# Kernel optimization log

Measured on AMD Instinct MI355X. Metric: run time of the kernel, lower is better.

The kernel has to match this reference:

```python
import jax, jax.numpy as jnp
import numpy as np

MUL = 50        # e3nn mul=50 channel multiplicity
LAYERS = 6      # layers=6
NBASIS = 10     # radial basis size
MAXR = 0.06     # max_radius
HIDDEN = 64     # radial MLP hidden
NPATHS = 5      # TP paths: s*Y0->s, s*Y1->v, v.Y1->s, vxY1->v, Y2@v->v
HALF_BAR = 0.05 # half bar length (bar lengths [0.1,0.1,0.1])


def setup_inputs() -> dict:
    key = jax.random.key(0)
    ks = jax.random.split(key, 9)
    B, L = 64, 514
    C = MUL
    y = jax.random.normal(ks[0], (B, L, 6), dtype=jnp.float32) * 0.03
    W_embed = jax.random.normal(ks[1], (3, C), dtype=jnp.float32) / np.sqrt(3.0)
    Wr1 = jax.random.normal(ks[2], (LAYERS, NBASIS + 2, HIDDEN), dtype=jnp.float32) / np.sqrt(NBASIS + 2.0)
    br1 = jnp.zeros((LAYERS, HIDDEN), dtype=jnp.float32)
    Wr2 = jax.random.normal(ks[3], (LAYERS, HIDDEN, NPATHS * C), dtype=jnp.float32) / np.sqrt(float(HIDDEN))
    Ws = jax.random.normal(ks[4], (LAYERS, C, C), dtype=jnp.float32) / np.sqrt(float(C))
    Wv = jax.random.normal(ks[5], (LAYERS, C, C), dtype=jnp.float32) / np.sqrt(float(C))
    Wg = jax.random.normal(ks[6], (LAYERS, C, C), dtype=jnp.float32) / np.sqrt(float(C))
    W_out = jax.random.normal(ks[7], (C,), dtype=jnp.float32) / np.sqrt(float(C))
    return {"y": y, "W_embed": W_embed, "Wr1": Wr1, "br1": br1, "Wr2": Wr2,
            "Ws": Ws, "Wv": Wv, "Wg": Wg, "W_out": W_out}


def _cross2d(a, b):
    return a[..., 0] * b[..., 1] - a[..., 1] * b[..., 0]


def _forward(y, W_embed, Wr1, br1, Wr2, Ws, Wv, Wg, W_out):
    B, L, _ = y.shape
    T = L - 2
    C = MUL
    # --- slinky coord transform: (x, z, alpha) dof -> 9 cartesian points/triplet ---
    ctr = jnp.stack([y[..., 0], y[..., 1]], axis=-1)                 # (B,L,2) bar centers
    a = y[..., 2]
    off = HALF_BAR * jnp.stack([-jnp.sin(a), jnp.cos(a)], axis=-1)   # (B,L,2)
    pts = jnp.stack([ctr + off, ctr, ctr - off], axis=-2)            # (B,L,3,2) top/center/bottom
    trip = jnp.stack([pts[:, :-2], pts[:, 1:-1], pts[:, 2:]], axis=2)  # (B,T,3bars,3pts,2)
    cart = trip.reshape(B * T, 9, 2)
    nt = B * T
    N = nt * 9
    pos = jnp.concatenate([cart.reshape(-1, 2), jnp.zeros((N, 1), cart.dtype)], axis=-1)  # (N,3)
    # --- fixed intra-triplet edge pattern ---
    base = jnp.array([[1, 0], [1, 2], [4, 3], [4, 5], [7, 6], [7, 8], [1, 4], [4, 7]], dtype=jnp.int32)
    eidx = (base[None] + 9 * jnp.arange(nt, dtype=jnp.int32)[:, None, None]).reshape(-1, 2)
    src, dst = eidx[:, 0], eidx[:, 1]
    edge_attr = jnp.tile(jax.nn.one_hot(jnp.array([1, 1, 1, 1, 1, 1, 0, 0]), 2, dtype=pos.dtype), (nt, 1))  # (E,2)
    node_attr = jnp.tile(jax.nn.one_hot(jnp.array([1, 0, 1]), 2, dtype=pos.dtype), (3 * nt, 1))             # (N,2)
    node_input = jnp.ones((N, 1), pos.dtype)
    # --- edge geometry: radial embedding + spherical harmonics l<=2 ---
    edge_vec = pos[src] - pos[dst]
    r = jnp.linalg.norm(edge_vec, axis=-1)
    u = edge_vec / (r[:, None] + 1e-12)                              # Y1 (l=1)
    centers = jnp.linspace(0.0, MAXR, NBASIS)
    width = MAXR / (NBASIS - 1)
    rb = jnp.exp(-jnp.square((r[:, None] - centers) / width))        # (E,NBASIS)
    t = jnp.clip(r / MAXR, 0.0, 1.0)
    fcut = 0.5 * (jnp.cos(jnp.float32(np.pi) * t) + 1.0)             # smooth cutoff at max_radius
    emb = jnp.concatenate([rb * fcut[:, None], edge_attr], axis=-1)  # (E,NBASIS+2)
    Y2 = u[:, :, None] * u[:, None, :] - jnp.eye(3, dtype=u.dtype) / 3.0  # traceless l=2 (E,3,3)
    # --- node feature init: scalars (0e) + zero vectors (1o) ---
    s = jnp.concatenate([node_input, node_attr], axis=-1) @ W_embed  # (N,C)
    v = jnp.zeros((N, C, 3), pos.dtype)
    for l in range(LAYERS):
        w = jax.nn.silu(emb @ Wr1[l] + br1[l]) @ Wr2[l]              # radial MLP -> TP weights
        w = w.reshape(-1, NPATHS, C) * fcut[:, None, None]           # (E,5,C)
        ss, vs = s[src], v[src]
        m_s = w[:, 0] * ss + w[:, 2] * jnp.einsum('ecd,ed->ec', vs, u)
        m_v = (w[:, 1, :, None] * ss[:, :, None] * u[:, None, :]
               + w[:, 3, :, None] * jnp.cross(vs, u[:, None, :])
               + w[:, 4, :, None] * jnp.einsum('ecd,edk->eck', vs, Y2))
        s_agg = jax.ops.segment_sum(m_s, dst, num_segments=N)        # scatter-add (num_neighbors=1)
        v_agg = jax.ops.segment_sum(m_v, dst, num_segments=N)
        h = s + s_agg
        s = jax.nn.silu(h @ Ws[l])                                   # scalar nonlinearity
        gate = jax.nn.sigmoid(h @ Wg[l])                             # equivariant gate for vectors
        v = jnp.einsum('ncd,ck->nkd', v + v_agg, Wv[l]) * gate[:, :, None]
    out = jnp.einsum('ncd,c->nd', v, W_out)                          # 1x1o readout, (N,3)
    output = out.reshape(B, T, 3, 3, 3)                              # (B,T,bar,point,xyz)
    cart_b = cart.reshape(B, T, 3, 3, 2)
    result = jnp.zeros((B, L, 3), y.dtype)
    result = result.at[:, 1:-1, 0:2].set(output.sum(axis=-2)[..., 1, 0:2])
    tmp = (_cross2d(cart_b[..., 0, :] - cart_b[..., 1, :], output[..., 0, 0:2])
           + _cross2d(cart_b[..., 2, :] - cart_b[..., 1, :], output[..., 2, 0:2]))
    result = result.at[:, 1:-1, 2].set(tmp[..., 1])
    return result


def reference(y, W_embed, Wr1, br1, Wr2, Ws, Wv, Wg, W_out):
    return _forward(y, W_embed, Wr1, br1, Wr2, Ws, Wv, Wg, W_out)
```

## Files before the change

### kernel.cpp

```cpp
#include <hip/hip_runtime.h>
#include <math.h>

#define PI_F 3.14159265358979323846f

typedef _Float16 h8 __attribute__((ext_vector_type(8)));
typedef float f4 __attribute__((ext_vector_type(4)));

__device__ __forceinline__ float sigm_(float x){ return 1.0f/(1.0f+__expf(-x)); }
__device__ __forceinline__ float silu_(float x){ return x*sigm_(x); }
__device__ __forceinline__ h8 ldh8(const _Float16* p){
    return __builtin_bit_cast(h8, *(const float4*)(p));
}

#define B1_PER_L 21504
#define B2_PER_L 12288
#define B1_TOT   129024
#define B_TOT    202752

__global__ void precompute_all(const float* __restrict__ W_embed,
                               const float* __restrict__ Wr1,
                               const float* __restrict__ br1,
                               const float* __restrict__ Wr2,
                               const float* __restrict__ Ws,
                               const float* __restrict__ Wg,
                               const float* __restrict__ Wv,
                               float* __restrict__ pre,
                               float* __restrict__ T,
                               int tabN,
                               _Float16* __restrict__ B,
                               float* __restrict__ out,
                               int nTb)
{
    const int bid = blockIdx.x;
    const int tid = threadIdx.x;
    const float wdt = 0.06f / 9.0f;

    if (bid == 0) {
        for (int i = tid; i < 384; i += 256) {
            int b = i / 6, r = i - b * 6;
            int t = (r < 3) ? 0 : 513;
            out[((size_t)(b * 514 + t)) * 3 + (r % 3)] = 0.0f;
        }
        __shared__ float s1[50];
        __shared__ float hid[64];
        if (tid < 50) s1[tid] = W_embed[tid] + W_embed[50 + tid];
        __syncthreads();

        const float rbar = 0.05f;
        const float fcb = 0.5f * (__cosf(PI_F * (rbar / 0.06f)) + 1.0f);
        float emb[12];
#pragma unroll
        for (int i = 0; i < 10; ++i) {
            float d = (rbar - (float)i * wdt) / wdt;
            emb[i] = __expf(-d * d) * fcb;
        }
        emb[10] = 0.0f; emb[11] = 1.0f;

        for (int l = 0; l < 6; ++l) {
            if (tid < 50) pre[l * 50 + tid] = s1[tid];
            if (tid < 64) {
                float a = br1[l * 64 + tid];
#pragma unroll
                for (int i = 0; i < 12; ++i) a += emb[i] * Wr1[l * 768 + i * 64 + tid];
                hid[tid] = silu_(a);
            }
            __syncthreads();
            for (int m = tid; m < 250; m += 256) {
                float acc = 0.0f;
                for (int j = 0; j < 64; ++j) acc += hid[j] * Wr2[l * 16000 + j * 250 + m];
                pre[300 + l * 250 + m] = acc * fcb;
            }
            float sacc = 0.0f;
            if (tid < 50) {
                for (int c = 0; c < 50; ++c) sacc += s1[c] * Ws[l * 2500 + c * 50 + tid];
            }
            __syncthreads();
            if (tid < 50) s1[tid] = silu_(sacc);
            __syncthreads();
        }
    } else if (bid <= nTb) {
        const int e = (bid - 1) * 4 + (tid >> 6);
        const int lane = tid & 63;
        const int total = 6 * (tabN + 1);
        if (e >= total) return;
        const int l = e / (tabN + 1);
        const int i = e - l * (tabN + 1);

        float r = (float)i * (0.06f / (float)tabN);
        float t = fminf(r * (1.0f / 0.06f), 1.0f);
        float fc = 0.5f * (__cosf(PI_F * t) + 1.0f);
        float emb[10];
#pragma unroll
        for (int k = 0; k < 10; ++k) {
            float d = (r - (float)k * wdt) / wdt;
            emb[k] = __expf(-d * d) * fc;
        }
        float a = br1[l * 64 + lane] + Wr1[l * 768 + 640 + lane];
#pragma unroll
        for (int k = 0; k < 10; ++k) a += emb[k] * Wr1[l * 768 + k * 64 + lane];
        float hv = silu_(a);

        float acc0 = 0.0f, acc1 = 0.0f;
        const float* wr2 = Wr2 + l * 16000;
        for (int j = 0; j < 64; ++j) {
            float hj = __shfl(hv, j);
            acc0 += hj * wr2[j * 250 + lane];
            acc1 += hj * wr2[j * 250 + 64 + lane];
        }
        float* tp = T + (size_t)e * 100;
        tp[lane] = acc0 * fc;
        if (lane < 36) tp[64 + lane] = acc1 * fc;
    } else {
        int idx = (bid - 1 - nTb) * 256 + tid;
        if (idx >= B_TOT) return;
        int l, n, k, which;
        size_t off;
        if (idx < B1_TOT) {
            l = idx / B1_PER_L; int r = idx - l * B1_PER_L;
            n = r / 192; k = r - n * 192; which = 0;
            off = (size_t)l * B1_PER_L + n * 192 + k;
        } else {
            int j = idx - B1_TOT;
            l = j / B2_PER_L; int r = j - l * B2_PER_L;
            n = r / 192; k = r - n * 192; which = 1;
            off = B1_TOT + (size_t)l * B2_PER_L + n * 192 + k;
        }
        int seg = -1, c = 0;
        if (k < 50)                  { seg = 0; c = k; }
        else if (k >= 64 && k < 114) { seg = 1; c = k - 64; }
        else if (k >= 128 && k < 178){ seg = 2; c = k - 128; }
        _Float16 val = (_Float16)0.0f;
        if (seg >= 0) {
            float w = 0.0f;
            if (which == 0) {
                if (n < 50)       w = Ws[l * 2500 + c * 50 + n];
                else if (n < 100) w = Wg[l * 2500 + c * 50 + (n - 50)];
            } else {
                if (n < 50)       w = Wv[l * 2500 + c * 50 + n];
            }
            _Float16 hi = (_Float16)w;
            val = (seg < 2) ? hi : (_Float16)(w - (float)hi);
        }
        B[off] = val;
    }
}

__global__ __launch_bounds__(256, 4)
void fused_main(const float* __restrict__ y,
                const float* __restrict__ W_embed,
                const float* __restrict__ W_out,
                const float* __restrict__ pre,
                const float* __restrict__ T,
                int tabN,
                const _Float16* __restrict__ Bws,
                float* __restrict__ out)
{
    __shared__ __align__(16) char LB[112 * 152 * 2];
    _Float16* A   = (_Float16*)LB;
    float* outHT  = (float*)LB;
    float* outQT  = (float*)LB + 3200;

    const int tid  = threadIdx.x;
    const int wave = tid >> 6;
    const int lane = tid & 63;
    const int kl   = (lane < 50) ? lane : 49;
    const int fm   = lane & 15;
    const int fq   = lane >> 4;

    const _Float16* B1 = Bws;
    const _Float16* B2 = Bws + B1_TOT;

    float offx[2], offy[2], u3x_[2], u3y_[2], uspx_[2], uspy_[2], fr_[2];
    int   ti_[2], inr_[2];
#pragma unroll
    for (int w = 0; w < 2; ++w) {
        int wid = blockIdx.x * 8 + wave * 2 + w;
        int b = wid >> 9, tw = wid & 511;
        const float* yb = y + ((size_t)(b * 514 + tw)) * 6;
        float c0x = yb[0], c0y = yb[1];
        float c1x = yb[6], c1y = yb[7], a1 = yb[8];
        float sn, cs; __sincosf(a1, &sn, &cs);
        offx[w] = -0.05f * sn; offy[w] = 0.05f * cs;
        float svx = c0x - c1x, svy = c0y - c1y;
        float r_sp = sqrtf(svx * svx + svy * svy);
        float inv_sp = 1.0f / (r_sp + 1e-12f);
        uspx_[w] = svx * inv_sp; uspy_[w] = svy * inv_sp;
        float rb2 = sqrtf(offx[w] * offx[w] + offy[w] * offy[w]);
        float invb = 1.0f / (rb2 + 1e-12f);
        u3x_[w] = -offx[w] * invb; u3y_[w] = -offy[w] * invb;
        float tp = r_sp * ((float)tabN / 0.06f);
        inr_[w] = tp < (float)tabN;
        int ti = (int)tp;
        if (ti > tabN - 1) ti = tabN - 1;
        if (ti < 0) ti = 0;
        ti_[w] = ti; fr_[w] = tp - (float)ti;
    }

    float s3[2], s4[2], s5[2];
    float v3x[2], v3y[2], v3z[2], v4x[2], v4y[2], v4z[2], v5x[2], v5y[2], v5z[2];
    {
        float i35 = W_embed[kl] + W_embed[100 + kl];
        float i4  = W_embed[kl] + W_embed[50 + kl];
#pragma unroll
        for (int w = 0; w < 2; ++w) {
            s3[w] = i35; s5[w] = i35; s4[w] = i4;
            v3x[w] = v3y[w] = v3z[w] = 0.0f;
            v4x[w] = v4y[w] = v4z[w] = 0.0f;
            v5x[w] = v5y[w] = v5z[w] = 0.0f;
        }
    }

    for (int l = 0; l < 6; ++l) {
        __syncthreads();

        float s1l = pre[l * 50 + kl];
        const float* wbp = pre + 300 + l * 250;
        float wb0 = wbp[kl], wb1 = wbp[50 + kl], wb2 = wbp[100 + kl],
              wb3 = wbp[150 + kl], wb4 = wbp[200 + kl];

        const float THIRD = 1.0f / 3.0f;
#pragma unroll
        for (int w = 0; w < 2; ++w) {
            const float* tb = T + ((size_t)(l * (tabN + 1) + ti_[w])) * 100;
            float t00 = tb[kl], t01 = tb[50 + kl], t10 = tb[100 + kl], t11 = tb[150 + kl];
            float wsp0 = inr_[w] ? (t00 + fr_[w] * (t10 - t00)) : 0.0f;
            float wsp1 = inr_[w] ? (t01 + fr_[w] * (t11 - t01)) : 0.0f;

            float u3x = u3x_[w], u3y = u3y_[w];
            float dot3 = v4x[w] * u3x + v4y[w] * u3y;
            float ms3 = wb0 * s4[w] + wb2 * dot3;
            float ms5 = wb0 * s4[w] - wb2 * dot3;
            float ms4 = wsp0 * s1l;
            float bAx = wb1 * s4[w] * u3x - wb3 * v4z[w] * u3y;
            float bAy = wb1 * s4[w] * u3y + wb3 * v4z[w] * u3x;
            float bBx = wb4 * (dot3 * u3x - v4x[w] * THIRD);
            float bBy = wb4 * (dot3 * u3y - v4y[w] * THIRD);
            float crz = wb3 * (v4x[w] * u3y - v4y[w] * u3x);
            float mzc = -wb4 * v4z[w] * THIRD;

            float vals[12];
            vals[0] = s3[w] + ms3;
            vals[1] = s4[w] + ms4;
            vals[2] = s5[w] + ms5;
            vals[3] = v3x[w] + bAx + bBx;
            vals[4] = v3y[w] + bAy + bBy;
            vals[5] = v3z[w] + crz + mzc;
            vals[6] = v4x[w] + wsp1 * s1l * uspx_[w];
            vals[7] = v4y[w] + wsp1 * s1l * uspy_[w];
            vals[8] = v4z[w];
            vals[9]  = v5x[w] - bAx + bBx;
            vals[10] = v5y[w] - bAy + bBy;
            vals[11] = v5z[w] - crz + mzc;

            int wv = wave * 2 + w;
#pragma unroll
            for (int q = 0; q < 12; ++q) {
                int row = (q < 3) ? (wv * 3 + q) : (32 + wv * 9 + (q - 3));
                float x = (lane < 50) ? vals[q] : 0.0f;
                _Float16 hi = (_Float16)x;
                _Float16 lo = (_Float16)(x - (float)hi);
                A[row * 152 + lane]      = hi;
                A[row * 152 + 64 + lane] = lo;
            }
        }
        {
            int pr  = tid >> 4;
            int row = (pr < 8) ? (24 + pr) : (96 + pr);
            f4 z = {0.0f, 0.0f, 0.0f, 0.0f};
            *(f4*)(A + row * 152 + (tid & 15) * 8) = z;
        }
        __syncthreads();

        f4 cst[9];
        const _Float16* B1l = B1 + (size_t)l * B1_PER_L;
        const _Float16* B2l = B2 + (size_t)l * B2_PER_L;

        {
            const _Float16* bp = B1l + (wave * 16 + fm) * 192 + fq * 8;
            h8 b0 = ldh8(bp), b1 = ldh8(bp + 32), b2 = ldh8(bp + 64),
               b3 = ldh8(bp + 96), b4 = ldh8(bp + 128), b5 = ldh8(bp + 160);
#pragma unroll
            for (int mt = 0; mt < 2; ++mt) {
                const _Float16* ap = A + (mt * 16 + fm) * 152 + fq * 8;
                h8 a0 = ldh8(ap), a1 = ldh8(ap + 32), a2 = ldh8(ap + 64), a3 = ldh8(ap + 96);
                f4 acc = {0.0f, 0.0f, 0.0f, 0.0f};
                acc = __builtin_amdgcn_mfma_f32_16x16x32_f16(a0, b0, acc, 0, 0, 0);
                acc = __builtin_amdgcn_mfma_f32_16x16x32_f16(a1, b1, acc, 0, 0, 0);
                acc = __builtin_amdgcn_mfma_f32_16x16x32_f16(a2, b2, acc, 0, 0, 0);
                acc = __builtin_amdgcn_mfma_f32_16x16x32_f16(a3, b3, acc, 0, 0, 0);
                acc = __builtin_amdgcn_mfma_f32_16x16x32_f16(a0, b4, acc, 0, 0, 0);
                acc = __builtin_amdgcn_mfma_f32_16x16x32_f16(a1, b5, acc, 0, 0, 0);
                cst[mt] = acc;
            }
        }
        if (wave < 3) {
            const _Float16* bp = B1l + ((4 + wave) * 16 + fm) * 192 + fq * 8;
            h8 b0 = ldh8(bp), b1 = ldh8(bp + 32), b2 = ldh8(bp + 64),
               b3 = ldh8(bp + 96), b4 = ldh8(bp + 128), b5 = ldh8(bp + 160);
#pragma unroll
            for (int mt = 0; mt < 2; ++mt) {
                const _Float16* ap = A + (mt * 16 + fm) * 152 + fq * 8;
                h8 a0 = ldh8(ap), a1 = ldh8(ap + 32), a2 = ldh8(ap + 64), a3 = ldh8(ap + 96);
                f4 acc = {0.0f, 0.0f, 0.0f, 0.0f};
                acc = __builtin_amdgcn_mfma_f32_16x16x32_f16(a0, b0, acc, 0, 0, 0);
                acc = __builtin_amdgcn_mfma_f32_16x16x32_f16(a1, b1, acc, 0, 0, 0);
                acc = __builtin_amdgcn_mfma_f32_16x16x32_f16(a2, b2, acc, 0, 0, 0);
                acc = __builtin_amdgcn_mfma_f32_16x16x32_f16(a3, b3, acc, 0, 0, 0);
                acc = __builtin_amdgcn_mfma_f32_16x16x32_f16(a0, b4, acc, 0, 0, 0);
                acc = __builtin_amdgcn_mfma_f32_16x16x32_f16(a1, b5, acc, 0, 0, 0);
                cst[2 + mt] = acc;
            }
        }
        {
            const _Float16* bp = B2l + (wave * 16 + fm) * 192 + fq * 8;
            h8 b0 = ldh8(bp), b1 = ldh8(bp + 32), b2 = ldh8(bp + 64),
               b3 = ldh8(bp + 96), b4 = ldh8(bp + 128), b5 = ldh8(bp + 160);
#pragma unroll
            for (int mt = 0; mt < 5; ++mt) {
                const _Float16* ap = A + (32 + mt * 16 + fm) * 152 + fq * 8;
                h8 a0 = ldh8(ap), a1 = ldh8(ap + 32), a2 = ldh8(ap + 64), a3 = ldh8(ap + 96);
                f4 acc = {0.0f, 0.0f, 0.0f, 0.0f};
                acc = __builtin_amdgcn_mfma_f32_16x16x32_f16(a0, b0, acc, 0, 0, 0);
                acc = __builtin_amdgcn_mfma_f32_16x16x32_f16(a1, b1, acc, 0, 0, 0);
                acc = __builtin_amdgcn_mfma_f32_16x16x32_f16(a2, b2, acc, 0, 0, 0);
                acc = __builtin_amdgcn_mfma_f32_16x16x32_f16(a3, b3, acc, 0, 0, 0);
                acc = __builtin_amdgcn_mfma_f32_16x16x32_f16(a0, b4, acc, 0, 0, 0);
                acc = __builtin_amdgcn_mfma_f32_16x16x32_f16(a1, b5, acc, 0, 0, 0);
                cst[4 + mt] = acc;
            }
        }
        __syncthreads();

        {
            int n0 = wave * 16 + fm;
#pragma unroll
            for (int mt = 0; mt < 2; ++mt)
#pragma unroll
                for (int i = 0; i < 4; ++i)
                    outHT[(mt * 16 + fq * 4 + i) * 100 + n0] = cst[mt][i];
            if (wave < 3) {
                int n1 = (4 + wave) * 16 + fm;
                if (n1 < 100) {
#pragma unroll
                    for (int mt = 0; mt < 2; ++mt)
#pragma unroll
                        for (int i = 0; i < 4; ++i)
                            outHT[(mt * 16 + fq * 4 + i) * 100 + n1] = cst[2 + mt][i];
                }
            }
            if (n0 < 50) {
#pragma unroll
                for (int mt = 0; mt < 5; ++mt)
#pragma unroll
                    for (int i = 0; i < 4; ++i)
                        outQT[(mt * 16 + fq * 4 + i) * 50 + n0] = cst[4 + mt][i];
            }
        }
        __syncthreads();

#pragma unroll
        for (int w = 0; w < 2; ++w) {
            int wv = wave * 2 + w;
            int mb = wv * 3, qb = wv * 9;
            float as3 = outHT[(mb    ) * 100 + kl];
            float as4 = outHT[(mb + 1) * 100 + kl];
            float as5 = outHT[(mb + 2) * 100 + kl];
            float ag3 = outHT[(mb    ) * 100 + 50 + kl];
            float ag4 = outHT[(mb + 1) * 100 + 50 + kl];
            float ag5 = outHT[(mb + 2) * 100 + 50 + kl];
            float g3 = sigm_(ag3), g4 = sigm_(ag4), g5 = sigm_(ag5);
            s3[w] = silu_(as3); s4[w] = silu_(as4); s5[w] = silu_(as5);
            v3x[w] = outQT[(qb    ) * 50 + kl] * g3;
            v3y[w] = outQT[(qb + 1) * 50 + kl] * g3;
            v3z[w] = outQT[(qb + 2) * 50 + kl] * g3;
            v4x[w] = outQT[(qb + 3) * 50 + kl] * g4;
            v4y[w] = outQT[(qb + 4) * 50 + kl] * g4;
            v4z[w] = outQT[(qb + 5) * 50 + kl] * g4;
            v5x[w] = outQT[(qb + 6) * 50 + kl] * g5;
            v5y[w] = outQT[(qb + 7) * 50 + kl] * g5;
            v5z[w] = outQT[(qb + 8) * 50 + kl] * g5;
        }
    }

    float wo = (lane < 50) ? W_out[lane] : 0.0f;
#pragma unroll
    for (int w = 0; w < 2; ++w) {
        float px  = (v3x[w] + v4x[w] + v5x[w]) * wo;
        float py  = (v3y[w] + v4y[w] + v5y[w]) * wo;
        float dxv = (v3x[w] - v5x[w]) * wo;
        float dyv = (v3y[w] - v5y[w]) * wo;
#pragma unroll
        for (int o = 32; o > 0; o >>= 1) {
            px  += __shfl_xor(px, o);
            py  += __shfl_xor(py, o);
            dxv += __shfl_xor(dxv, o);
            dyv += __shfl_xor(dyv, o);
        }
        if (lane == 0) {
            int wid = blockIdx.x * 8 + wave * 2 + w;
            int b = wid >> 9, tw = wid & 511;
            float* op = out + ((size_t)(b * 514 + (tw + 1))) * 3;
            op[0] = px;
            op[1] = py;
            op[2] = offx[w] * dyv - offy[w] * dxv;
        }
    }
}

extern "C" void kernel_launch(void* const* d_in, const int* in_sizes, int n_in,
                              void* d_out, int out_size, void* d_ws, size_t ws_size,
                              hipStream_t stream) {
    const float* y       = (const float*)d_in[0];
    const float* W_embed = (const float*)d_in[1];
    const float* Wr1     = (const float*)d_in[2];
    const float* br1     = (const float*)d_in[3];
    const float* Wr2     = (const float*)d_in[4];
    const float* Ws      = (const float*)d_in[5];
    const float* Wv      = (const float*)d_in[6];
    const float* Wg      = (const float*)d_in[7];
    const float* W_out   = (const float*)d_in[8];
    float* out = (float*)d_out;

    _Float16* Bws = (_Float16*)d_ws;
    float* pre = (float*)((char*)d_ws + B_TOT * 2);
    float* T   = pre + 1800;

    int tabN = 2048;
    while (tabN > 64 &&
           (size_t)B_TOT * 2 + (size_t)(1800 + 6 * (tabN + 1) * 100) * sizeof(float) > ws_size)
        tabN >>= 1;

    int nTb = (6 * (tabN + 1) + 3) / 4;
    int nFb = (B_TOT + 255) / 256;
    precompute_all<<<1 + nTb + nFb, 256, 0, stream>>>(
        W_embed, Wr1, br1, Wr2, Ws, Wg, Wv, pre, T, tabN, Bws, out, nTb);
    fused_main<<<4096, 256, 0, stream>>>(y, W_embed, W_out, pre, T, tabN, Bws, out);
}
```

Baseline: 300.9 us.

## Prefetch next-layer tables and MFMA weights, interleave table layout, shrink LDS stride

Loads the B-operand weight fragments at the top of each layer, before the LDS fill and barrier, so global latency overlaps the A-tile construction. The radial table and per-layer coefficients for the next layer are software-prefetched into registers. The table is stored with the two path weights interleaved so each lane reads a float2. The kernel also shrinks the LDS row stride to 136, raises the occupancy hint to 5 blocks, and halves the table resolution. Together these raise register pressure and may change LDS bank behavior, and the coarser table may reduce interpolation accuracy.

```diff
diff --git a/kernel.cpp b/kernel.cpp
--- a/kernel.cpp
+++ b/kernel.cpp
@@ -16,6 +16,8 @@
 #define B2_PER_L 12288
 #define B1_TOT   129024
 #define B_TOT    202752
+
+#define ASTR 136
 
 __global__ void precompute_all(const float* __restrict__ W_embed,
                                const float* __restrict__ Wr1,
@@ -108,8 +110,10 @@
             acc1 += hj * wr2[j * 250 + 64 + lane];
         }
         float* tp = T + (size_t)e * 100;
-        tp[lane] = acc0 * fc;
-        if (lane < 36) tp[64 + lane] = acc1 * fc;
+        float sh0 = __shfl(acc0, lane + 50);
+        float sh1 = __shfl(acc1, lane - 14);
+        float vb = ((lane < 14) ? sh0 : sh1) * fc;
+        if (lane < 50) *(float2*)(tp + 2 * lane) = make_float2(acc0 * fc, vb);
     } else {
         int idx = (bid - 1 - nTb) * 256 + tid;
         if (idx >= B_TOT) return;
@@ -145,7 +149,7 @@
     }
 }
 
-__global__ __launch_bounds__(256, 4)
+__global__ __launch_bounds__(256, 5)
 void fused_main(const float* __restrict__ y,
                 const float* __restrict__ W_embed,
                 const float* __restrict__ W_out,
@@ -155,7 +159,7 @@
                 const _Float16* __restrict__ Bws,
                 float* __restrict__ out)
 {
-    __shared__ __align__(16) char LB[112 * 152 * 2];
+    __shared__ __align__(16) char LB[112 * ASTR * 2];
     _Float16* A   = (_Float16*)LB;
     float* outHT  = (float*)LB;
     float* outQT  = (float*)LB + 3200;
@@ -210,33 +214,72 @@
         }
     }
 
+    float2 tc0[2], tc1[2];
+    float s1c, w0c, w1c, w2c, w3c, w4c;
+#pragma unroll
+    for (int w = 0; w < 2; ++w) {
+        const float* tb = T + (size_t)ti_[w] * 100 + 2 * kl;
+        tc0[w] = *(const float2*)tb;
+        tc1[w] = *(const float2*)(tb + 100);
+    }
+    s1c = pre[kl];
+    {
+        const float* wq = pre + 300;
+        w0c = wq[kl]; w1c = wq[50 + kl]; w2c = wq[100 + kl];
+        w3c = wq[150 + kl]; w4c = wq[200 + kl];
+    }
+
     for (int l = 0; l < 6; ++l) {
         __syncthreads();
 
-        float s1l = pre[l * 50 + kl];
-        const float* wbp = pre + 300 + l * 250;
-        float wb0 = wbp[kl], wb1 = wbp[50 + kl], wb2 = wbp[100 + kl],
-              wb3 = wbp[150 + kl], wb4 = wbp[200 + kl];
+        const _Float16* B1l = B1 + (size_t)l * B1_PER_L;
+        const _Float16* B2l = B2 + (size_t)l * B2_PER_L;
+        const _Float16* bpA = B1l + (wave * 16 + fm) * 192 + fq * 8;
+        h8 bA0 = ldh8(bpA), bA1 = ldh8(bpA + 32), bA2 = ldh8(bpA + 64),
+           bA3 = ldh8(bpA + 96), bA4 = ldh8(bpA + 128), bA5 = ldh8(bpA + 160);
+        h8 bB0, bB1, bB2, bB3, bB4, bB5;
+        if (wave < 3) {
+            const _Float16* bpB = B1l + ((4 + wave) * 16 + fm) * 192 + fq * 8;
+            bB0 = ldh8(bpB); bB1 = ldh8(bpB + 32); bB2 = ldh8(bpB + 64);
+            bB3 = ldh8(bpB + 96); bB4 = ldh8(bpB + 128); bB5 = ldh8(bpB + 160);
+        }
+        const _Float16* bpC = B2l + (wave * 16 + fm) * 192 + fq * 8;
+        h8 bC0 = ldh8(bpC), bC1 = ldh8(bpC + 32), bC2 = ldh8(bpC + 64),
+           bC3 = ldh8(bpC + 96), bC4 = ldh8(bpC + 128), bC5 = ldh8(bpC + 160);
+
+        float2 tn0[2], tn1[2];
+        float s1n, w0n, w1n, w2n, w3n, w4n;
+        if (l < 5) {
+#pragma unroll
+            for (int w = 0; w < 2; ++w) {
+                const float* tb = T + ((size_t)((l + 1) * (tabN + 1) + ti_[w])) * 100 + 2 * kl;
+                tn0[w] = *(const float2*)tb;
+                tn1[w] = *(const float2*)(tb + 100);
+            }
+            const float* pp = pre + (l + 1) * 50;
+            s1n = pp[kl];
+            const float* wq = pre + 300 + (l + 1) * 250;
+            w0n = wq[kl]; w1n = wq[50 + kl]; w2n = wq[100 + kl];
+            w3n = wq[150 + kl]; w4n = wq[200 + kl];
+        }
 
         const float THIRD = 1.0f / 3.0f;
 #pragma unroll
         for (int w = 0; w < 2; ++w) {
-            const float* tb = T + ((size_t)(l * (tabN + 1) + ti_[w])) * 100;
-            float t00 = tb[kl], t01 = tb[50 + kl], t10 = tb[100 + kl], t11 = tb[150 + kl];
-            float wsp0 = inr_[w] ? (t00 + fr_[w] * (t10 - t00)) : 0.0f;
-            float wsp1 = inr_[w] ? (t01 + fr_[w] * (t11 - t01)) : 0.0f;
+            float wsp0 = inr_[w] ? (tc0[w].x + fr_[w] * (tc1[w].x - tc0[w].x)) : 0.0f;
+            float wsp1 = inr_[w] ? (tc0[w].y + fr_[w] * (tc1[w].y - tc0[w].y)) : 0.0f;
 
             float u3x = u3x_[w], u3y = u3y_[w];
             float dot3 = v4x[w] * u3x + v4y[w] * u3y;
-            float ms3 = wb0 * s4[w] + wb2 * dot3;
-            float ms5 = wb0 * s4[w] - wb2 * dot3;
-            float ms4 = wsp0 * s1l;
-            float bAx = wb1 * s4[w] * u3x - wb3 * v4z[w] * u3y;
-            float bAy = wb1 * s4[w] * u3y + wb3 * v4z[w] * u3x;
-            float bBx = wb4 * (dot3 * u3x - v4x[w] * THIRD);
-            float bBy = wb4 * (dot3 * u3y - v4y[w] * THIRD);
-            float crz = wb3 * (v4x[w] * u3y - v4y[w] * u3x);
-            float mzc = -wb4 * v4z[w] * THIRD;
+            float ms3 = w0c * s4[w] + w2c * dot3;
+            float ms5 = w0c * s4[w] - w2c * dot3;
+            float ms4 = wsp0 * s1c;
+            float bAx = w1c * s4[w] * u3x - w3c * v4z[w] * u3y;
+            float bAy = w1c * s4[w] * u3y + w3c * v4z[w] * u3x;
+            float bBx = w4c * (dot3 * u3x - v4x[w] * THIRD);
+            float bBy = w4c * (dot3 * u3y - v4y[w] * THIRD);
+            float crz = w3c * (v4x[w] * u3y - v4y[w] * u3x);
+            float mzc = -w4c * v4z[w] * THIRD;
 
             float vals[12];
             vals[0] = s3[w] + ms3;
@@ -245,8 +288,8 @@
             vals[3] = v3x[w] + bAx + bBx;
             vals[4] = v3y[w] + bAy + bBy;
             vals[5] = v3z[w] + crz + mzc;
-            vals[6] = v4x[w] + wsp1 * s1l * uspx_[w];
-            vals[7] = v4y[w] + wsp1 * s1l * uspy_[w];
+            vals[6] = v4x[w] + wsp1 * s1c * uspx_[w];
+            vals[7] = v4y[w] + wsp1 * s1c * uspy_[w];
             vals[8] = v4z[w];
             vals[9]  = v5x[w] - bAx + bBx;
             vals[10] = v5y[w] - bAy + bBy;
@@ -259,75 +302,54 @@
                 float x = (lane < 50) ? vals[q] : 0.0f;
                 _Float16 hi = (_Float16)x;
                 _Float16 lo = (_Float16)(x - (float)hi);
-                A[row * 152 + lane]      = hi;
-                A[row * 152 + 64 + lane] = lo;
+                A[row * ASTR + lane]      = hi;
+                A[row * ASTR + 64 + lane] = lo;
             }
         }
         {
             int pr  = tid >> 4;
             int row = (pr < 8) ? (24 + pr) : (96 + pr);
             f4 z = {0.0f, 0.0f, 0.0f, 0.0f};
-            *(f4*)(A + row * 152 + (tid & 15) * 8) = z;
+            *(f4*)(A + row * ASTR + (tid & 15) * 8) = z;
         }
         __syncthreads();
 
         f4 cst[9];
-        const _Float16* B1l = B1 + (size_t)l * B1_PER_L;
-        const _Float16* B2l = B2 + (size_t)l * B2_PER_L;
-
-        {
-            const _Float16* bp = B1l + (wave * 16 + fm) * 192 + fq * 8;
-            h8 b0 = ldh8(bp), b1 = ldh8(bp + 32), b2 = ldh8(bp + 64),
-               b3 = ldh8(bp + 96), b4 = ldh8(bp + 128), b5 = ldh8(bp + 160);
-#pragma unroll
-            for (int mt = 0; mt < 2; ++mt) {
-                const _Float16* ap = A + (mt * 16 + fm) * 152 + fq * 8;
-                h8 a0 = ldh8(ap), a1 = ldh8(ap + 32), a2 = ldh8(ap + 64), a3 = ldh8(ap + 96);
-                f4 acc = {0.0f, 0.0f, 0.0f, 0.0f};
-                acc = __builtin_amdgcn_mfma_f32_16x16x32_f16(a0, b0, acc, 0, 0, 0);
-                acc = __builtin_amdgcn_mfma_f32_16x16x32_f16(a1, b1, acc, 0, 0, 0);
-                acc = __builtin_amdgcn_mfma_f32_16x16x32_f16(a2, b2, acc, 0, 0, 0);
-                acc = __builtin_amdgcn_mfma_f32_16x16x32_f16(a3, b3, acc, 0, 0, 0);
-                acc = __builtin_amdgcn_mfma_f32_16x16x32_f16(a0, b4, acc, 0, 0, 0);
-                acc = __builtin_amdgcn_mfma_f32_16x16x32_f16(a1, b5, acc, 0, 0, 0);
-                cst[mt] = acc;
-            }
-        }
-        if (wave < 3) {
-            const _Float16* bp = B1l + ((4 + wave) * 16 + fm) * 192 + fq * 8;
-            h8 b0 = ldh8(bp), b1 = ldh8(bp + 32), b2 = ldh8(bp + 64),
-               b3 = ldh8(bp + 96), b4 = ldh8(bp + 128), b5 = ldh8(bp + 160);
-#pragma unroll
-            for (int mt = 0; mt < 2; ++mt) {
-                const _Float16* ap = A + (mt * 16 + fm) * 152 + fq * 8;
-                h8 a0 = ldh8(ap), a1 = ldh8(ap + 32), a2 = ldh8(ap + 64), a3 = ldh8(ap + 96);
-                f4 acc = {0.0f, 0.0f, 0.0f, 0.0f};
-                acc = __builtin_amdgcn_mfma_f32_16x16x32_f16(a0, b0, acc, 0, 0, 0);
-                acc = __builtin_amdgcn_mfma_f32_16x16x32_f16(a1, b1, acc, 0, 0, 0);
-                acc = __builtin_amdgcn_mfma_f32_16x16x32_f16(a2, b2, acc, 0, 0, 0);
-                acc = __builtin_amdgcn_mfma_f32_16x16x32_f16(a3, b3, acc, 0, 0, 0);
-                acc = __builtin_amdgcn_mfma_f32_16x16x32_f16(a0, b4, acc, 0, 0, 0);
-                acc = __builtin_amdgcn_mfma_f32_16x16x32_f16(a1, b5, acc, 0, 0, 0);
-                cst[2 + mt] = acc;
-            }
-        }
-        {
-            const _Float16* bp = B2l + (wave * 16 + fm) * 192 + fq * 8;
-            h8 b0 = ldh8(bp), b1 = ldh8(bp + 32), b2 = ldh8(bp + 64),
-               b3 = ldh8(bp + 96), b4 = ldh8(bp + 128), b5 = ldh8(bp + 160);
-#pragma unroll
-            for (int mt = 0; mt < 5; ++mt) {
-                const _Float16* ap = A + (32 + mt * 16 + fm) * 152 + fq * 8;
-                h8 a0 = ldh8(ap), a1 = ldh8(ap + 32), a2 = ldh8(ap + 64), a3 = ldh8(ap + 96);
-                f4 acc = {0.0f, 0.0f, 0.0f, 0.0f};
-                acc = __builtin_amdgcn_mfma_f32_16x16x32_f16(a0, b0, acc, 0, 0, 0);
-                acc = __builtin_amdgcn_mfma_f32_16x16x32_f16(a1, b1, acc, 0, 0, 0);
-                acc = __builtin_amdgcn_mfma_f32_16x16x32_f16(a2, b2, acc, 0, 0, 0);
-                acc = __builtin_amdgcn_mfma_f32_16x16x32_f16(a3, b3, acc, 0, 0, 0);
-                acc = __builtin_amdgcn_mfma_f32_16x16x32_f16(a0, b4, acc, 0, 0, 0);
-                acc = __builtin_amdgcn_mfma_f32_16x16x32_f16(a1, b5, acc, 0, 0, 0);
-                cst[4 + mt] = acc;
-            }
+#pragma unroll
+        for (int mt = 0; mt < 2; ++mt) {
+            const _Float16* ap = A + (mt * 16 + fm) * ASTR + fq * 8;
+            h8 a0 = ldh8(ap), a1 = ldh8(ap + 32), a2 = ldh8(ap + 64), a3 = ldh8(ap + 96);
+            f4 acc = {0.0f, 0.0f, 0.0f, 0.0f};
+            acc = __builtin_amdgcn_mfma_f32_16x16x32_f16(a0, bA0, acc, 0, 0, 0);
+            acc = __builtin_amdgcn_mfma_f32_16x16x32_f16(a1, bA1, acc, 0, 0, 0);
+            acc = __builtin_amdgcn_mfma_f32_16x16x32_f16(a2, bA2, acc, 0, 0, 0);
+            acc = __builtin_amdgcn_mfma_f32_16x16x32_f16(a3, bA3, acc, 0, 0, 0);
+            acc = __builtin_amdgcn_mfma_f32_16x16x32_f16(a0, bA4, acc, 0, 0, 0);
+            acc = __builtin_amdgcn_mfma_f32_16x16x32_f16(a1, bA5, acc, 0, 0, 0);
+            cst[mt] = acc;
+            if (wave < 3) {
+                f4 acc2 = {0.0f, 0.0f, 0.0f, 0.0f};
+                acc2 = __builtin_amdgcn_mfma_f32_16x16x32_f16(a0, bB0, acc2, 0, 0, 0);
+                acc2 = __builtin_amdgcn_mfma_f32_16x16x32_f16(a1, bB1, acc2, 0, 0, 0);
+                acc2 = __builtin_amdgcn_mfma_f32_16x16x32_f16(a2, bB2, acc2, 0, 0, 0);
+                acc2 = __builtin_amdgcn_mfma_f32_16x16x32_f16(a3, bB3, acc2, 0, 0, 0);
+                acc2 = __builtin_amdgcn_mfma_f32_16x16x32_f16(a0, bB4, acc2, 0, 0, 0);
+                acc2 = __builtin_amdgcn_mfma_f32_16x16x32_f16(a1, bB5, acc2, 0, 0, 0);
+                cst[2 + mt] = acc2;
+            }
+        }
+#pragma unroll
+        for (int mt = 0; mt < 5; ++mt) {
+            const _Float16* ap = A + (32 + mt * 16 + fm) * ASTR + fq * 8;
+            h8 a0 = ldh8(ap), a1 = ldh8(ap + 32), a2 = ldh8(ap + 64), a3 = ldh8(ap + 96);
+            f4 acc = {0.0f, 0.0f, 0.0f, 0.0f};
+            acc = __builtin_amdgcn_mfma_f32_16x16x32_f16(a0, bC0, acc, 0, 0, 0);
+            acc = __builtin_amdgcn_mfma_f32_16x16x32_f16(a1, bC1, acc, 0, 0, 0);
+            acc = __builtin_amdgcn_mfma_f32_16x16x32_f16(a2, bC2, acc, 0, 0, 0);
+            acc = __builtin_amdgcn_mfma_f32_16x16x32_f16(a3, bC3, acc, 0, 0, 0);
+            acc = __builtin_amdgcn_mfma_f32_16x16x32_f16(a0, bC4, acc, 0, 0, 0);
+            acc = __builtin_amdgcn_mfma_f32_16x16x32_f16(a1, bC5, acc, 0, 0, 0);
+            cst[4 + mt] = acc;
         }
         __syncthreads();
 
@@ -380,6 +402,12 @@
             v5y[w] = outQT[(qb + 7) * 50 + kl] * g5;
             v5z[w] = outQT[(qb + 8) * 50 + kl] * g5;
         }
+
+        if (l < 5) {
+            tc0[0] = tn0[0]; tc0[1] = tn0[1];
+            tc1[0] = tn1[0]; tc1[1] = tn1[1];
+            s1c = s1n; w0c = w0n; w1c = w1n; w2c = w2n; w3c = w3n; w4c = w4n;
+        }
     }
 
     float wo = (lane < 50) ? W_out[lane] : 0.0f;
@@ -425,7 +453,7 @@
     float* pre = (float*)((char*)d_ws + B_TOT * 2);
     float* T   = pre + 1800;
 
-    int tabN = 2048;
+    int tabN = 1024;
     while (tabN > 64 &&
            (size_t)B_TOT * 2 + (size_t)(1800 + 6 * (tabN + 1) * 100) * sizeof(float) > ws_size)
         tabN >>= 1;
```

Result: slower. 617.9 us (+105.3%).

## Compact and swizzle LDS A-tile, interleave radial table, raise occupancy

Applied to the files above, without the earlier changes.

Shrinks the shared A tile from 112x152 to 104x128 halves using an XOR swizzle instead of padding, and drops the zero-fill of padding rows. Rows that overlap between the H and Q tiles are masked on write-back. Interleaves the two radial-table channels so each lookup is one float2 load, and halves the table size. Launch bounds are raised to 6 blocks per CU so the smaller LDS footprint can give more occupancy, at the cost of register pressure and coarser radial interpolation.

```diff
diff --git a/kernel.cpp b/kernel.cpp
--- a/kernel.cpp
+++ b/kernel.cpp
@@ -16,6 +16,8 @@
 #define B2_PER_L 12288
 #define B1_TOT   129024
 #define B_TOT    202752
+
+#define AROWS 104
 
 __global__ void precompute_all(const float* __restrict__ W_embed,
                                const float* __restrict__ Wr1,
@@ -108,8 +110,10 @@
             acc1 += hj * wr2[j * 250 + 64 + lane];
         }
         float* tp = T + (size_t)e * 100;
-        tp[lane] = acc0 * fc;
-        if (lane < 36) tp[64 + lane] = acc1 * fc;
+        float sh0 = __shfl(acc0, lane + 50);
+        float sh1 = __shfl(acc1, lane - 14);
+        float vb = ((lane < 14) ? sh0 : sh1) * fc;
+        if (lane < 50) *(float2*)(tp + 2 * lane) = make_float2(acc0 * fc, vb);
     } else {
         int idx = (bid - 1 - nTb) * 256 + tid;
         if (idx >= B_TOT) return;
@@ -145,7 +149,7 @@
     }
 }
 
-__global__ __launch_bounds__(256, 4)
+__global__ __launch_bounds__(256, 6)
 void fused_main(const float* __restrict__ y,
                 const float* __restrict__ W_embed,
                 const float* __restrict__ W_out,
@@ -155,10 +159,10 @@
                 const _Float16* __restrict__ Bws,
                 float* __restrict__ out)
 {
-    __shared__ __align__(16) char LB[112 * 152 * 2];
+    __shared__ __align__(16) char LB[AROWS * 128 * 2];
     _Float16* A   = (_Float16*)LB;
     float* outHT  = (float*)LB;
-    float* outQT  = (float*)LB + 3200;
+    float* outQT  = (float*)LB + 2400;
 
     const int tid  = threadIdx.x;
     const int wave = tid >> 6;
@@ -169,6 +173,15 @@
 
     const _Float16* B1 = Bws;
     const _Float16* B2 = Bws + B1_TOT;
+
+    auto lda = [&](int row, h8& a0, h8& a1, h8& a2, h8& a3) {
+        const int base = row * 128 + ((fq ^ (row & 3)) << 3);
+        const int x32  = ((row >> 2) & 1) << 5;
+        a0 = ldh8(A + base + x32);
+        a1 = ldh8(A + base + (32 - x32));
+        a2 = ldh8(A + base + 64 + x32);
+        a3 = ldh8(A + base + 96 - x32);
+    };
 
     float offx[2], offy[2], u3x_[2], u3y_[2], uspx_[2], uspy_[2], fr_[2];
     int   ti_[2], inr_[2];
@@ -221,10 +234,11 @@
         const float THIRD = 1.0f / 3.0f;
 #pragma unroll
         for (int w = 0; w < 2; ++w) {
-            const float* tb = T + ((size_t)(l * (tabN + 1) + ti_[w])) * 100;
-            float t00 = tb[kl], t01 = tb[50 + kl], t10 = tb[100 + kl], t11 = tb[150 + kl];
-            float wsp0 = inr_[w] ? (t00 + fr_[w] * (t10 - t00)) : 0.0f;
-            float wsp1 = inr_[w] ? (t01 + fr_[w] * (t11 - t01)) : 0.0f;
+            const float* tb = T + ((size_t)(l * (tabN + 1) + ti_[w])) * 100 + 2 * kl;
+            float2 t0 = *(const float2*)tb;
+            float2 t1 = *(const float2*)(tb + 100);
+            float wsp0 = inr_[w] ? (t0.x + fr_[w] * (t1.x - t0.x)) : 0.0f;
+            float wsp1 = inr_[w] ? (t0.y + fr_[w] * (t1.y - t0.y)) : 0.0f;
 
             float u3x = u3x_[w], u3y = u3y_[w];
             float dot3 = v4x[w] * u3x + v4y[w] * u3y;
@@ -255,19 +269,14 @@
             int wv = wave * 2 + w;
 #pragma unroll
             for (int q = 0; q < 12; ++q) {
-                int row = (q < 3) ? (wv * 3 + q) : (32 + wv * 9 + (q - 3));
+                int row = (q < 3) ? (wv * 3 + q) : (24 + wv * 9 + (q - 3));
                 float x = (lane < 50) ? vals[q] : 0.0f;
                 _Float16 hi = (_Float16)x;
                 _Float16 lo = (_Float16)(x - (float)hi);
-                A[row * 152 + lane]      = hi;
-                A[row * 152 + 64 + lane] = lo;
-            }
-        }
-        {
-            int pr  = tid >> 4;
-            int row = (pr < 8) ? (24 + pr) : (96 + pr);
-            f4 z = {0.0f, 0.0f, 0.0f, 0.0f};
-            *(f4*)(A + row * 152 + (tid & 15) * 8) = z;
+                int col = lane ^ ((row & 7) << 3);
+                A[row * 128 + col]      = hi;
+                A[row * 128 + col + 64] = lo;
+            }
         }
         __syncthreads();
 
@@ -281,8 +290,8 @@
                b3 = ldh8(bp + 96), b4 = ldh8(bp + 128), b5 = ldh8(bp + 160);
 #pragma unroll
             for (int mt = 0; mt < 2; ++mt) {
-                const _Float16* ap = A + (mt * 16 + fm) * 152 + fq * 8;
-                h8 a0 = ldh8(ap), a1 = ldh8(ap + 32), a2 = ldh8(ap + 64), a3 = ldh8(ap + 96);
+                h8 a0, a1, a2, a3;
+                lda(mt * 16 + fm, a0, a1, a2, a3);
                 f4 acc = {0.0f, 0.0f, 0.0f, 0.0f};
                 acc = __builtin_amdgcn_mfma_f32_16x16x32_f16(a0, b0, acc, 0, 0, 0);
                 acc = __builtin_amdgcn_mfma_f32_16x16x32_f16(a1, b1, acc, 0, 0, 0);
@@ -299,8 +308,8 @@
                b3 = ldh8(bp + 96), b4 = ldh8(bp + 128), b5 = ldh8(bp + 160);
 #pragma unroll
             for (int mt = 0; mt < 2; ++mt) {
-                const _Float16* ap = A + (mt * 16 + fm) * 152 + fq * 8;
-                h8 a0 = ldh8(ap), a1 = ldh8(ap + 32), a2 = ldh8(ap + 64), a3 = ldh8(ap + 96);
+                h8 a0, a1, a2, a3;
+                lda(mt * 16 + fm, a0, a1, a2, a3);
                 f4 acc = {0.0f, 0.0f, 0.0f, 0.0f};
                 acc = __builtin_amdgcn_mfma_f32_16x16x32_f16(a0, b0, acc, 0, 0, 0);
                 acc = __builtin_amdgcn_mfma_f32_16x16x32_f16(a1, b1, acc, 0, 0, 0);
@@ -317,8 +326,8 @@
                b3 = ldh8(bp + 96), b4 = ldh8(bp + 128), b5 = ldh8(bp + 160);
 #pragma unroll
             for (int mt = 0; mt < 5; ++mt) {
-                const _Float16* ap = A + (32 + mt * 16 + fm) * 152 + fq * 8;
-                h8 a0 = ldh8(ap), a1 = ldh8(ap + 32), a2 = ldh8(ap + 64), a3 = ldh8(ap + 96);
+                h8 a0, a1, a2, a3;
+                lda(24 + mt * 16 + fm, a0, a1, a2, a3);
                 f4 acc = {0.0f, 0.0f, 0.0f, 0.0f};
                 acc = __builtin_amdgcn_mfma_f32_16x16x32_f16(a0, b0, acc, 0, 0, 0);
                 acc = __builtin_amdgcn_mfma_f32_16x16x32_f16(a1, b1, acc, 0, 0, 0);
@@ -336,24 +345,30 @@
 #pragma unroll
             for (int mt = 0; mt < 2; ++mt)
 #pragma unroll
-                for (int i = 0; i < 4; ++i)
-                    outHT[(mt * 16 + fq * 4 + i) * 100 + n0] = cst[mt][i];
+                for (int i = 0; i < 4; ++i) {
+                    int r = mt * 16 + fq * 4 + i;
+                    if (r < 24) outHT[r * 100 + n0] = cst[mt][i];
+                }
             if (wave < 3) {
                 int n1 = (4 + wave) * 16 + fm;
                 if (n1 < 100) {
 #pragma unroll
                     for (int mt = 0; mt < 2; ++mt)
 #pragma unroll
-                        for (int i = 0; i < 4; ++i)
-                            outHT[(mt * 16 + fq * 4 + i) * 100 + n1] = cst[2 + mt][i];
+                        for (int i = 0; i < 4; ++i) {
+                            int r = mt * 16 + fq * 4 + i;
+                            if (r < 24) outHT[r * 100 + n1] = cst[2 + mt][i];
+                        }
                 }
             }
             if (n0 < 50) {
 #pragma unroll
                 for (int mt = 0; mt < 5; ++mt)
 #pragma unroll
-                    for (int i = 0; i < 4; ++i)
-                        outQT[(mt * 16 + fq * 4 + i) * 50 + n0] = cst[4 + mt][i];
+                    for (int i = 0; i < 4; ++i) {
+                        int r = mt * 16 + fq * 4 + i;
+                        if (r < 72) outQT[r * 50 + n0] = cst[4 + mt][i];
+                    }
             }
         }
         __syncthreads();
@@ -425,7 +440,7 @@
     float* pre = (float*)((char*)d_ws + B_TOT * 2);
     float* T   = pre + 1800;
 
-    int tabN = 2048;
+    int tabN = 1024;
     while (tabN > 64 &&
            (size_t)B_TOT * 2 + (size_t)(1800 + 6 * (tabN + 1) * 100) * sizeof(float) > ws_size)
         tabN >>= 1;
```

Result: slower. 587.0 us (+95.1%).
